# Kernel optimization log

Measured on AMD Instinct MI355X. Metric: run time of the kernel, lower is better.

## Reference

```python
import jax, jax.numpy as jnp
import numpy as np

N, E, D, R = 50000, 800000, 64, 65


def setup_inputs() -> dict:
    key = jax.random.key(0)
    ks = jax.random.split(key, 8)
    x = jax.random.normal(ks[0], (N, D), dtype=jnp.float32)
    src = jax.random.randint(ks[1], (E,), 0, N, dtype=jnp.int32)
    dst = jax.random.randint(ks[2], (E,), 0, N, dtype=jnp.int32)
    edge_type = jax.random.randint(ks[3], (E,), 0, R, dtype=jnp.int32)
    s = 1.0 / np.sqrt(D)
    W1 = jax.random.normal(ks[4], (R, D, D), dtype=jnp.float32) * s
    Wl1 = jax.random.normal(ks[5], (D, D), dtype=jnp.float32) * s
    W2 = jax.random.normal(ks[6], (R, D, D), dtype=jnp.float32) * s
    Wl2 = jax.random.normal(ks[7], (D, D), dtype=jnp.float32) * s
    return {"x": x, "src": src, "dst": dst, "edge_type": edge_type,
            "W1": W1, "Wl1": Wl1, "W2": W2, "Wl2": Wl2}


def _rgcn_layer(x, src, dst, edge_type, W, Wl):
    # x: [N, D_in], W: [R, D_in, D_out], Wl: [D_in, D_out]
    n = x.shape[0]
    r = W.shape[0]
    # per-relation transform of all node features: [R, N, D_out]
    xw = jnp.einsum('nd,rdh->rnh', x, W)
    # gather transformed source feature for each edge by its relation: [E, D_out]
    msg = xw[edge_type, src]
    # mean aggregation per (destination node, relation) as in PyG RGCNConv
    key = dst.astype(jnp.int32) * r + edge_type
    cnt = jax.ops.segment_sum(jnp.ones(key.shape, x.dtype), key, num_segments=n * r)
    norm = 1.0 / jnp.maximum(cnt[key], 1.0)  # [E]
    agg = jax.ops.segment_sum(msg * norm[:, None], dst, num_segments=n)  # [N, D_out]
    # self-loop linear term (self_loop_weights in original module)
    out = agg + x @ Wl
    # activation; dropout is identity in eval mode; batch norm disabled
    return jax.nn.relu(out)


def reference(x, src, dst, edge_type, W1, Wl1, W2, Wl2):
    h = _rgcn_layer(x, src, dst, edge_type, W1, Wl1)
    h = _rgcn_layer(h, src, dst, edge_type, W2, Wl2)
    return h
```

## Files before the change

kernel.cpp:

```cpp
#include <hip/hip_runtime.h>

typedef __attribute__((ext_vector_type(8))) short bf16x8;
typedef __attribute__((ext_vector_type(4))) float f32x4;
typedef __attribute__((ext_vector_type(2))) unsigned int u32x2;

constexpr int D = 64;
constexpr int SEG = 64;
constexpr int CSTR = 16;
constexpr int SBS = 1024;

__device__ inline unsigned short f2bf(float f) {
  unsigned u = __float_as_uint(f);
  u += 0x7fff + ((u >> 16) & 1);
  return (unsigned short)(u >> 16);
}
__device__ inline float bflo(unsigned u) { return __uint_as_float(u << 16); }
__device__ inline float bfhi(unsigned u) { return __uint_as_float(u & 0xffff0000u); }

__global__ __launch_bounds__(SBS) void count_kernel(
    const int* __restrict__ dst, const int* __restrict__ et,
    int* __restrict__ bcnt, int* __restrict__ deg, int E, int R, int nbE) {
  __shared__ int lh[128];
  int t = threadIdx.x;
  if (t < 128) lh[t] = 0;
  __syncthreads();
  int e = blockIdx.x * SBS + t;
  if (e < E) {
    atomicAdd(&deg[(long)dst[e] * CSTR], 1);
    atomicAdd(&lh[et[e]], 1);
  }
  __syncthreads();
  if (t < R) bcnt[t * nbE + blockIdx.x] = lh[t];
}

__global__ __launch_bounds__(256) void scanA_dual_kernel(
    const int* __restrict__ bcnt, const int* __restrict__ deg,
    int* __restrict__ bsum, int nBC, int N, int nbBC) {
  __shared__ int s[256];
  int t = threadIdx.x;
  int b = blockIdx.x;
  int v;
  if (b < nbBC) {
    int i = b * 256 + t;
    v = (i < nBC) ? bcnt[i] : 0;
  } else {
    int i = (b - nbBC) * 256 + t;
    v = (i < N) ? deg[(long)i * CSTR] : 0;
  }
  s[t] = v;
  __syncthreads();
  for (int o = 128; o > 0; o >>= 1) {
    if (t < o) s[t] += s[t + o];
    __syncthreads();
  }
  if (t == 0) bsum[b] = s[0];
}

__device__ inline void scanB_region(int* bsum, int nb, int t) {
  __shared__ int s[256];
  __shared__ int carry;
  if (t == 0) carry = 0;
  __syncthreads();
  for (int base = 0; base < nb; base += 256) {
    int i = base + t;
    int v = (i < nb) ? bsum[i] : 0;
    s[t] = v;
    __syncthreads();
    for (int o = 1; o < 256; o <<= 1) {
      int u = (t >= o) ? s[t - o] : 0;
      __syncthreads();
      s[t] += u;
      __syncthreads();
    }
    if (i < nb) bsum[i] = carry + s[t] - v;
    __syncthreads();
    if (t == 0) carry += s[255];
    __syncthreads();
  }
}

__global__ __launch_bounds__(256) void scanB_dual_kernel(
    int* __restrict__ bsum, int nbBC, int nbN) {
  int t = threadIdx.x;
  scanB_region(bsum, nbBC, t);
  scanB_region(bsum + nbBC, nbN, t);
}

__global__ __launch_bounds__(256) void scanC_dual_kernel(
    const int* __restrict__ bcnt, const int* __restrict__ deg,
    const int* __restrict__ bsum, int* __restrict__ prefE,
    int* __restrict__ dstoff, int* __restrict__ cur2,
    int nBC, int N, int nbBC) {
  __shared__ int s[256];
  int t = threadIdx.x;
  int b = blockIdx.x;
  bool isBC = (b < nbBC);
  int i = (isBC ? b : b - nbBC) * 256 + t;
  int n = isBC ? nBC : N;
  int v = 0;
  if (i < n) v = isBC ? bcnt[i] : deg[(long)i * CSTR];
  s[t] = v;
  __syncthreads();
  for (int o = 1; o < 256; o <<= 1) {
    int u = (t >= o) ? s[t - o] : 0;
    __syncthreads();
    s[t] += u;
    __syncthreads();
  }
  int excl = bsum[b] + s[t] - v;
  if (isBC) {
    if (i < n) prefE[i] = excl;
    if (i == n - 1) prefE[n] = excl + v;
  } else {
    if (i < n) { dstoff[i] = excl; cur2[(long)i * CSTR] = excl; }
    if (i == n - 1) dstoff[n] = excl + v;
  }
}

__global__ void prefix_wrel_kernel(const int* __restrict__ prefE,
                                   int* __restrict__ cursor, int* __restrict__ wrel,
                                   int2* __restrict__ eidx,
                                   int nbE, int R, int Ecap, int nwavesTot) {
  __shared__ int sc[128];
  int l = threadIdx.x;
  int tot = 0, c = 0;
  if (l < R) {
    tot = prefE[(l + 1) * nbE] - prefE[l * nbE];
    c = (tot + SEG - 1) & ~(SEG - 1);
  }
  sc[l] = c;
  __syncthreads();
  for (int ofs = 1; ofs < 128; ofs <<= 1) {
    int v = (l >= ofs) ? sc[l - ofs] : 0;
    __syncthreads();
    sc[l] += v;
    __syncthreads();
  }
  if (l < R) {
    int cur = sc[l] - c;
    cursor[l] = cur;
    int w0 = cur >> 6;
    int nw = c >> 6;
    for (int w = 0; w < nw; ++w) wrel[w0 + w] = l;
    for (int p = cur + tot; p < cur + c; ++p) eidx[p] = make_int2(-1, -1);
  }
  int total = sc[127];
  for (int p = total + l; p < Ecap; p += 128) eidx[p] = make_int2(-1, -1);
  for (int w = (total >> 6) + l; w < nwavesTot; w += 128) wrel[w] = 0;
}

__global__ __launch_bounds__(SBS) void scatter_kernel(
    const int* __restrict__ src, const int* __restrict__ dst, const int* __restrict__ et,
    const int* __restrict__ cursor, const int* __restrict__ prefE,
    int* __restrict__ cur2, int2* __restrict__ eidx,
    int E, int R, int nbE) {
  __shared__ int lh[128];
  __shared__ int lbase[128];
  __shared__ int lpre[128];
  __shared__ int sv[SBS];
  __shared__ int jv[SBS];
  __shared__ int rv[SBS];
  int t = threadIdx.x, b = blockIdx.x;
  if (t < 128) {
    lh[t] = 0;
    lbase[t] = (t < R) ? (cursor[t] + prefE[t * nbE + b] - prefE[t * nbE]) : 0;
  }
  __syncthreads();
  int e = b * SBS + t;
  bool valid = (e < E);
  int r = 0, s = 0, jd = 0, lr = 0;
  if (valid) {
    r = et[e]; s = src[e]; int d = dst[e];
    lr = atomicAdd(&lh[r], 1);
    jd = atomicAdd(&cur2[(long)d * CSTR], 1);
  }
  __syncthreads();
  if (t < 128) lpre[t] = lh[t];
  __syncthreads();
  for (int o = 1; o < 128; o <<= 1) {
    int u = (t >= o && t < 128) ? lpre[t - o] : 0;
    __syncthreads();
    if (t < 128) lpre[t] += u;
    __syncthreads();
  }
  if (valid) {
    int slot = (lpre[r] - lh[r]) + lr;
    sv[slot] = s; jv[slot] = jd; rv[slot] = r;
  }
  __syncthreads();
  int nvalid = min(E - b * SBS, SBS);
  if (t < nvalid) {
    int rr = rv[t];
    int ex = lpre[rr] - lh[rr];
    int pos = lbase[rr] + (t - ex);
    eidx[pos] = make_int2(sv[t], jv[t]);
  }
}

__global__ __launch_bounds__(256) void cvt_kernel(
    const float* __restrict__ x, unsigned short* __restrict__ xb, int nx, int nxb,
    const float* __restrict__ W1, unsigned short* __restrict__ WT1,
    const float* __restrict__ W2, unsigned short* __restrict__ WT2,
    const float* __restrict__ Wl1, unsigned short* __restrict__ WTl1,
    const float* __restrict__ Wl2, unsigned short* __restrict__ WTl2, int R) {
  const int b = blockIdx.x;
  const int t = threadIdx.x;
  if (b < nxb) {
    long i = ((long)b * 256 + t) * 8;
    if (i < nx) {
      float4 f0 = *(const float4*)(x + i);
      float4 f1 = *(const float4*)(x + i + 4);
      bf16x8 o;
      o[0] = (short)f2bf(f0.x); o[1] = (short)f2bf(f0.y);
      o[2] = (short)f2bf(f0.z); o[3] = (short)f2bf(f0.w);
      o[4] = (short)f2bf(f1.x); o[5] = (short)f2bf(f1.y);
      o[6] = (short)f2bf(f1.z); o[7] = (short)f2bf(f1.w);
      *(bf16x8*)(xb + i) = o;
    }
    return;
  }
  const int m = b - nxb;
  const float* Wsrc;
  unsigned short* Wdst;
  if (m < R)          { Wsrc = W1 + ((long)m << 12);        Wdst = WT1 + ((long)m << 12); }
  else if (m < 2 * R) { Wsrc = W2 + ((long)(m - R) << 12);  Wdst = WT2 + ((long)(m - R) << 12); }
  else if (m == 2 * R){ Wsrc = Wl1;                         Wdst = WTl1; }
  else                { Wsrc = Wl2;                         Wdst = WTl2; }
  __shared__ float tile[64][65];
#pragma unroll
  for (int it = 0; it < 16; ++it) {
    int idx = it * 256 + t;
    tile[idx >> 6][idx & 63] = Wsrc[idx];
  }
  __syncthreads();
#pragma unroll
  for (int it = 0; it < 16; ++it) {
    int j = it * 256 + t;
    Wdst[j] = f2bf(tile[j & 63][j >> 6]);
  }
}

__global__ __launch_bounds__(256)
void msg_kernel(const unsigned short* __restrict__ xb,
                const unsigned short* __restrict__ WT,
                const int2* __restrict__ eidx, const int* __restrict__ wrel,
                unsigned int* __restrict__ msgp, int* __restrict__ relrow, int nwaves) {
  const int lane = (int)threadIdx.x & 63;
  const int l15 = lane & 15;
  const int q = lane >> 4;
  const int nwg = (int)gridDim.x;
  const int bid = (int)blockIdx.x;
  const int xcd = bid & 7, idx = bid >> 3;
  const int qq = nwg >> 3, rr = nwg & 7;
  const int swz = (xcd < rr ? xcd * (qq + 1) : rr * (qq + 1) + (xcd - rr) * qq) + idx;
  const int wave = swz * 4 + ((int)threadIdx.x >> 6);
  if (wave >= nwaves) return;
  const long base = (long)wave * SEG;
  const int r = wrel[wave];
  const unsigned short* wb = WT + ((long)r << 12);
  int2 rec[4];
#pragma unroll
  for (int t = 0; t < 4; ++t) rec[t] = eidx[base + t * 16 + l15];
  bf16x8 Bf[4][2];
#pragma unroll
  for (int nt = 0; nt < 4; ++nt)
#pragma unroll
    for (int kh = 0; kh < 2; ++kh)
      Bf[nt][kh] = *(const bf16x8*)(wb + (nt * 16 + l15) * 64 + kh * 32 + q * 8);
  bf16x8 A[4][2];
#pragma unroll
  for (int t = 0; t < 4; ++t) {
    const unsigned short* xr = xb + ((long)max(rec[t].x, 0) << 6);
    A[t][0] = *(const bf16x8*)(xr + q * 8);
    A[t][1] = *(const bf16x8*)(xr + 32 + q * 8);
  }
  if (relrow) {
#pragma unroll
    for (int t = 0; t < 4; ++t)
      if (lane < 16 && rec[t].y >= 0) relrow[rec[t].y] = r;
  }
#pragma unroll
  for (int t = 0; t < 4; ++t) {
    f32x4 acc0 = (f32x4)0.0f, acc1 = (f32x4)0.0f, acc2 = (f32x4)0.0f, acc3 = (f32x4)0.0f;
    acc0 = __builtin_amdgcn_mfma_f32_16x16x32_bf16(A[t][0], Bf[0][0], acc0, 0, 0, 0);
    acc0 = __builtin_amdgcn_mfma_f32_16x16x32_bf16(A[t][1], Bf[0][1], acc0, 0, 0, 0);
    acc1 = __builtin_amdgcn_mfma_f32_16x16x32_bf16(A[t][0], Bf[1][0], acc1, 0, 0, 0);
    acc1 = __builtin_amdgcn_mfma_f32_16x16x32_bf16(A[t][1], Bf[1][1], acc1, 0, 0, 0);
    acc2 = __builtin_amdgcn_mfma_f32_16x16x32_bf16(A[t][0], Bf[2][0], acc2, 0, 0, 0);
    acc2 = __builtin_amdgcn_mfma_f32_16x16x32_bf16(A[t][1], Bf[2][1], acc2, 0, 0, 0);
    acc3 = __builtin_amdgcn_mfma_f32_16x16x32_bf16(A[t][0], Bf[3][0], acc3, 0, 0, 0);
    acc3 = __builtin_amdgcn_mfma_f32_16x16x32_bf16(A[t][1], Bf[3][1], acc3, 0, 0, 0);
#pragma unroll
    for (int rg = 0; rg < 4; ++rg) {
      int row = q * 4 + rg;
      int jd = __shfl(rec[t].y, row);
      if (jd >= 0) {
        unsigned p0 = (unsigned)f2bf(acc0[rg]) | ((unsigned)f2bf(acc1[rg]) << 16);
        unsigned p1 = (unsigned)f2bf(acc2[rg]) | ((unsigned)f2bf(acc3[rg]) << 16);
        u32x2 pk;
        pk.x = p0; pk.y = p1;
        *(u32x2*)(msgp + (long)jd * 32 + 2 * l15) = pk;
      }
    }
  }
}

__global__ __launch_bounds__(256) void weight_kernel(
    const int* __restrict__ relrow, const int* __restrict__ dstoff,
    float* __restrict__ wrow, int N) {
  __shared__ int rsh[4][256];
  const int wv = (int)threadIdx.x >> 6;
  const int lane = (int)threadIdx.x & 63;
  const int d = blockIdx.x * 4 + wv;
  if (d >= N) return;
  const int off = dstoff[d], end = dstoff[d + 1];
  const int deg = end - off;
  if (deg <= 0) return;
  if (deg <= 256) {
    const int nit = (deg + 63) >> 6;
    for (int it = 0; it < nit; ++it) {
      int l = it * 64 + lane;
      if (l < deg) rsh[wv][l] = relrow[off + l];
    }
    __threadfence_block();
    for (int it = 0; it < nit; ++it) {
      int l = it * 64 + lane;
      if (l < deg) {
        int rv = rsh[wv][l];
        int c = 0;
        for (int m = 0; m < deg; ++m) c += (rsh[wv][m] == rv) ? 1 : 0;
        wrow[off + l] = 1.0f / (float)c;
      }
    }
  } else {
    for (int l = lane; l < deg; l += 64) {
      int rv = relrow[off + l];
      int c = 0;
      for (int m = off; m < end; ++m) c += (relrow[m] == rv) ? 1 : 0;
      wrow[off + l] = 1.0f / (float)c;
    }
  }
}

__global__ __launch_bounds__(256) void aggsl_kernel(
    const unsigned int* __restrict__ msgp, const int* __restrict__ dstoff,
    const float* __restrict__ wrow,
    const unsigned short* __restrict__ xbin, const unsigned short* __restrict__ WTl,
    float* __restrict__ outp, unsigned short* __restrict__ hb, int N) {
  __shared__ float aggs[64][66];
  const int lane = (int)threadIdx.x & 63;
  const int wv = (int)threadIdx.x >> 6;
  const int base = blockIdx.x * 64;
  const int j = lane & 31;
  const int half = lane >> 5;
  for (int i16 = 0; i16 < 16; ++i16) {
    const int d = base + wv * 16 + i16;
    if (d >= N) break;
    const int off = dstoff[d], end = dstoff[d + 1];
    float a0 = 0.f, a1 = 0.f, b0 = 0.f, b1 = 0.f;
    float c0 = 0.f, c1 = 0.f, e0 = 0.f, e1 = 0.f;
    int i = off + half;
    for (; i + 6 < end; i += 8) {
      float w0 = wrow[i];
      float w1 = wrow[i + 2];
      float w2 = wrow[i + 4];
      float w3 = wrow[i + 6];
      unsigned u0 = msgp[(long)i * 32 + j];
      unsigned u1 = msgp[(long)(i + 2) * 32 + j];
      unsigned u2 = msgp[(long)(i + 4) * 32 + j];
      unsigned u3 = msgp[(long)(i + 6) * 32 + j];
      a0 = fmaf(w0, bflo(u0), a0);
      a1 = fmaf(w0, bfhi(u0), a1);
      b0 = fmaf(w1, bflo(u1), b0);
      b1 = fmaf(w1, bfhi(u1), b1);
      c0 = fmaf(w2, bflo(u2), c0);
      c1 = fmaf(w2, bfhi(u2), c1);
      e0 = fmaf(w3, bflo(u3), e0);
      e1 = fmaf(w3, bfhi(u3), e1);
    }
    for (; i + 2 < end; i += 4) {
      float w0 = wrow[i];
      float w1 = wrow[i + 2];
      unsigned u0 = msgp[(long)i * 32 + j];
      unsigned u1 = msgp[(long)(i + 2) * 32 + j];
      a0 = fmaf(w0, bflo(u0), a0);
      a1 = fmaf(w0, bfhi(u0), a1);
      b0 = fmaf(w1, bflo(u1), b0);
      b1 = fmaf(w1, bfhi(u1), b1);
    }
    if (i < end) {
      float w0 = wrow[i];
      unsigned u0 = msgp[(long)i * 32 + j];
      a0 = fmaf(w0, bflo(u0), a0);
      a1 = fmaf(w0, bfhi(u0), a1);
    }
    float aLo = (a0 + b0) + (c0 + e0), aHi = (a1 + b1) + (c1 + e1);
    aLo += __shfl_xor(aLo, 32);
    aHi += __shfl_xor(aHi, 32);
    if (half == 0) {
      const int k = j >> 1;
      const int colLo = (j & 1) ? 32 + k : k;
      aggs[d - base][colLo] = aLo;
      aggs[d - base][colLo + 16] = aHi;
    }
  }
  __syncthreads();
  const int l15 = lane & 15;
  const int q = lane >> 4;
  const int row0 = base + wv * 16;
  if (row0 >= N) return;
  bf16x8 Bf[4][2];
#pragma unroll
  for (int nt = 0; nt < 4; ++nt)
#pragma unroll
    for (int kh = 0; kh < 2; ++kh)
      Bf[nt][kh] = *(const bf16x8*)(WTl + (nt * 16 + l15) * 64 + kh * 32 + q * 8);
  const int m = min(row0 + l15, N - 1);
  const unsigned short* xr = xbin + ((long)m << 6);
  bf16x8 A0 = *(const bf16x8*)(xr + q * 8);
  bf16x8 A1 = *(const bf16x8*)(xr + 32 + q * 8);
  f32x4 acc[4];
#pragma unroll
  for (int nt = 0; nt < 4; ++nt)
#pragma unroll
    for (int rg = 0; rg < 4; ++rg) {
      int node = row0 + q * 4 + rg;
      acc[nt][rg] = (node < N) ? aggs[wv * 16 + q * 4 + rg][nt * 16 + l15] : 0.0f;
    }
#pragma unroll
  for (int nt = 0; nt < 4; ++nt) {
    acc[nt] = __builtin_amdgcn_mfma_f32_16x16x32_bf16(A0, Bf[nt][0], acc[nt], 0, 0, 0);
    acc[nt] = __builtin_amdgcn_mfma_f32_16x16x32_bf16(A1, Bf[nt][1], acc[nt], 0, 0, 0);
  }
#pragma unroll
  for (int rg = 0; rg < 4; ++rg) {
    int node = row0 + q * 4 + rg;
    if (node < N) {
#pragma unroll
      for (int nt = 0; nt < 4; ++nt) {
        float v = fmaxf(acc[nt][rg], 0.0f);
        if (outp) outp[(long)node * D + nt * 16 + l15] = v;
        if (hb) hb[(long)node * D + nt * 16 + l15] = f2bf(v);
      }
    }
  }
}

extern "C" void kernel_launch(void* const* d_in, const int* in_sizes, int n_in,
                              void* d_out, int out_size, void* d_ws, size_t ws_size,
                              hipStream_t stream) {
  const float* x   = (const float*)d_in[0];
  const int* src   = (const int*)d_in[1];
  const int* dst   = (const int*)d_in[2];
  const int* et    = (const int*)d_in[3];
  const float* W1  = (const float*)d_in[4];
  const float* Wl1 = (const float*)d_in[5];
  const float* W2  = (const float*)d_in[6];
  const float* Wl2 = (const float*)d_in[7];
  float* out = (float*)d_out;

  const int N = in_sizes[0] / D;
  const int E = in_sizes[1];
  const int R = in_sizes[4] / (D * D);

  const int Ecap = ((E + SEG - 1) & ~(SEG - 1)) + R * SEG;
  const int nwaves = Ecap / SEG;
  const int nbN = (N + 255) / 256;
  const int nbE = (E + SBS - 1) / SBS;
  const int nBC = R * nbE;
  const int nbBC = (nBC + 255) / 256;

  char* ws = (char*)d_ws;
  size_t off = 0;
  auto alloc = [&](size_t bytes) -> void* {
    void* p = (void*)(ws + off);
    off += (bytes + 255) & ~(size_t)255;
    return p;
  };
  int*   cursor = (int*)alloc((size_t)R * sizeof(int));
  int*   deg    = (int*)alloc((size_t)N * CSTR * sizeof(int));
  int*   cur2   = (int*)alloc((size_t)N * CSTR * sizeof(int));
  int*   bcnt   = (int*)alloc((size_t)nBC * sizeof(int));
  int*   prefE  = (int*)alloc((size_t)(nBC + 1) * sizeof(int));
  int*   bsum   = (int*)alloc((size_t)(nbBC + nbN) * sizeof(int));
  int*   dstoff = (int*)alloc((size_t)(N + 1) * sizeof(int));
  int*   relrow = (int*)alloc((size_t)E * sizeof(int));
  float* wrow   = (float*)alloc((size_t)E * sizeof(float));
  int*   wrel   = (int*)alloc((size_t)nwaves * sizeof(int));
  int2*  eidx   = (int2*)alloc((size_t)(Ecap + SEG) * sizeof(int2));
  unsigned int* msgp = (unsigned int*)alloc((size_t)E * 32 * sizeof(unsigned int));
  unsigned short* xb  = (unsigned short*)alloc((size_t)N * D * sizeof(unsigned short));
  unsigned short* hb  = (unsigned short*)alloc((size_t)N * D * sizeof(unsigned short));
  unsigned short* WT1 = (unsigned short*)alloc((size_t)R * D * D * sizeof(unsigned short));
  unsigned short* WT2 = (unsigned short*)alloc((size_t)R * D * D * sizeof(unsigned short));
  unsigned short* WTl1 = (unsigned short*)alloc((size_t)D * D * sizeof(unsigned short));
  unsigned short* WTl2 = (unsigned short*)alloc((size_t)D * D * sizeof(unsigned short));
  (void)ws_size; (void)n_in; (void)out_size;

  const int msg_blocks = (nwaves + 3) / 4;
  const int w_blocks = (N + 3) / 4;
  const int aggsl_blocks = (N + 63) / 64;
  const int nx = N * D;
  const int nxb = (nx + 2047) / 2048;
  const int cvt_blocks = nxb + 2 * R + 2;

  hipMemsetAsync(deg, 0, (size_t)N * CSTR * sizeof(int), stream);
  count_kernel<<<nbE, SBS, 0, stream>>>(dst, et, bcnt, deg, E, R, nbE);
  scanA_dual_kernel<<<nbBC + nbN, 256, 0, stream>>>(bcnt, deg, bsum, nBC, N, nbBC);
  scanB_dual_kernel<<<1, 256, 0, stream>>>(bsum, nbBC, nbN);
  scanC_dual_kernel<<<nbBC + nbN, 256, 0, stream>>>(bcnt, deg, bsum, prefE,
                                                    dstoff, cur2, nBC, N, nbBC);
  prefix_wrel_kernel<<<1, 128, 0, stream>>>(prefE, cursor, wrel, eidx,
                                            nbE, R, Ecap, nwaves);
  scatter_kernel<<<nbE, SBS, 0, stream>>>(src, dst, et, cursor, prefE, cur2,
                                          eidx, E, R, nbE);
  cvt_kernel<<<cvt_blocks, 256, 0, stream>>>(
      x, xb, nx, nxb, W1, WT1, W2, WT2, Wl1, WTl1, Wl2, WTl2, R);

  msg_kernel<<<msg_blocks, 256, 0, stream>>>(xb, WT1, eidx, wrel, msgp, relrow, nwaves);
  weight_kernel<<<w_blocks, 256, 0, stream>>>(relrow, dstoff, wrow, N);
  aggsl_kernel<<<aggsl_blocks, 256, 0, stream>>>(msgp, dstoff, wrow, xb, WTl1,
                                                 nullptr, hb, N);

  msg_kernel<<<msg_blocks, 256, 0, stream>>>(hb, WT2, eidx, wrel, msgp, nullptr, nwaves);
  aggsl_kernel<<<aggsl_blocks, 256, 0, stream>>>(msgp, dstoff, wrow, hb, WTl2,
                                                 out, nullptr, N);
}
```

Measured before the change: 326.9 us.

## Fuse setup kernels: merge count+convert, prefix into scatter, weights into aggregation

Folds the bf16 conversion of x and the weights into the count kernel launch, moves the per-relation prefix/wrel/padding setup into every scatter block (each block recomputes the scan redundantly), and computes the per-(dst,relation) mean weights inside the first aggregation kernel instead of a separate weight kernel. This removes three kernel launches and one pass over relrow/wrow. In exchange, every scatter block repeats a small scan, and the weight computation now sits on the aggregation critical path, where it adds shared memory use per block.

```diff
diff --git a/kernel.cpp b/kernel.cpp
--- a/kernel.cpp
+++ b/kernel.cpp
@@ -17,20 +17,63 @@
 __device__ inline float bflo(unsigned u) { return __uint_as_float(u << 16); }
 __device__ inline float bfhi(unsigned u) { return __uint_as_float(u & 0xffff0000u); }
 
-__global__ __launch_bounds__(SBS) void count_kernel(
+__global__ __launch_bounds__(SBS) void count_cvt_kernel(
     const int* __restrict__ dst, const int* __restrict__ et,
-    int* __restrict__ bcnt, int* __restrict__ deg, int E, int R, int nbE) {
-  __shared__ int lh[128];
+    int* __restrict__ bcnt, int* __restrict__ deg, int E, int R, int nbE,
+    const float* __restrict__ x, unsigned short* __restrict__ xb, int nx, int nxb,
+    const float* __restrict__ W1, unsigned short* __restrict__ WT1,
+    const float* __restrict__ W2, unsigned short* __restrict__ WT2,
+    const float* __restrict__ Wl1, unsigned short* __restrict__ WTl1,
+    const float* __restrict__ Wl2, unsigned short* __restrict__ WTl2) {
+  int b = blockIdx.x;
   int t = threadIdx.x;
-  if (t < 128) lh[t] = 0;
-  __syncthreads();
-  int e = blockIdx.x * SBS + t;
-  if (e < E) {
-    atomicAdd(&deg[(long)dst[e] * CSTR], 1);
-    atomicAdd(&lh[et[e]], 1);
-  }
-  __syncthreads();
-  if (t < R) bcnt[t * nbE + blockIdx.x] = lh[t];
+  if (b < nbE) {
+    __shared__ int lh[128];
+    if (t < 128) lh[t] = 0;
+    __syncthreads();
+    int e = b * SBS + t;
+    if (e < E) {
+      atomicAdd(&deg[(long)dst[e] * CSTR], 1);
+      atomicAdd(&lh[et[e]], 1);
+    }
+    __syncthreads();
+    if (t < R) bcnt[t * nbE + b] = lh[t];
+    return;
+  }
+  b -= nbE;
+  if (b < nxb) {
+    long i = ((long)b * SBS + t) * 8;
+    if (i < nx) {
+      float4 f0 = *(const float4*)(x + i);
+      float4 f1 = *(const float4*)(x + i + 4);
+      bf16x8 o;
+      o[0] = (short)f2bf(f0.x); o[1] = (short)f2bf(f0.y);
+      o[2] = (short)f2bf(f0.z); o[3] = (short)f2bf(f0.w);
+      o[4] = (short)f2bf(f1.x); o[5] = (short)f2bf(f1.y);
+      o[6] = (short)f2bf(f1.z); o[7] = (short)f2bf(f1.w);
+      *(bf16x8*)(xb + i) = o;
+    }
+    return;
+  }
+  const int m = b - nxb;
+  const float* Wsrc;
+  unsigned short* Wdst;
+  if (m < R)          { Wsrc = W1 + ((long)m << 12);        Wdst = WT1 + ((long)m << 12); }
+  else if (m < 2 * R) { Wsrc = W2 + ((long)(m - R) << 12);  Wdst = WT2 + ((long)(m - R) << 12); }
+  else if (m == 2 * R){ Wsrc = Wl1;                         Wdst = WTl1; }
+  else                { Wsrc = Wl2;                         Wdst = WTl2; }
+  __shared__ float tile[64][65];
+#pragma unroll
+  for (int it = 0; it < 4; ++it) {
+    int idx = it * SBS + t;
+    tile[idx >> 6][idx & 63] = Wsrc[idx];
+  }
+  __syncthreads();
+#pragma unroll
+  for (int it = 0; it < 4; ++it) {
+    int j = it * SBS + t;
+    Wdst[j] = f2bf(tile[j & 63][j >> 6]);
+  }
 }
 
 __global__ __launch_bounds__(256) void scanA_dual_kernel(
@@ -117,55 +160,55 @@
   }
 }
 
-__global__ void prefix_wrel_kernel(const int* __restrict__ prefE,
-                                   int* __restrict__ cursor, int* __restrict__ wrel,
-                                   int2* __restrict__ eidx,
-                                   int nbE, int R, int Ecap, int nwavesTot) {
-  __shared__ int sc[128];
-  int l = threadIdx.x;
-  int tot = 0, c = 0;
-  if (l < R) {
-    tot = prefE[(l + 1) * nbE] - prefE[l * nbE];
-    c = (tot + SEG - 1) & ~(SEG - 1);
-  }
-  sc[l] = c;
-  __syncthreads();
-  for (int ofs = 1; ofs < 128; ofs <<= 1) {
-    int v = (l >= ofs) ? sc[l - ofs] : 0;
-    __syncthreads();
-    sc[l] += v;
-    __syncthreads();
-  }
-  if (l < R) {
-    int cur = sc[l] - c;
-    cursor[l] = cur;
-    int w0 = cur >> 6;
-    int nw = c >> 6;
-    for (int w = 0; w < nw; ++w) wrel[w0 + w] = l;
-    for (int p = cur + tot; p < cur + c; ++p) eidx[p] = make_int2(-1, -1);
-  }
-  int total = sc[127];
-  for (int p = total + l; p < Ecap; p += 128) eidx[p] = make_int2(-1, -1);
-  for (int w = (total >> 6) + l; w < nwavesTot; w += 128) wrel[w] = 0;
-}
-
 __global__ __launch_bounds__(SBS) void scatter_kernel(
     const int* __restrict__ src, const int* __restrict__ dst, const int* __restrict__ et,
-    const int* __restrict__ cursor, const int* __restrict__ prefE,
-    int* __restrict__ cur2, int2* __restrict__ eidx,
-    int E, int R, int nbE) {
+    const int* __restrict__ prefE, int* __restrict__ cur2,
+    int2* __restrict__ eidx, int* __restrict__ wrel,
+    int E, int R, int nbE, int Ecap, int nwavesTot) {
   __shared__ int lh[128];
   __shared__ int lbase[128];
   __shared__ int lpre[128];
+  __shared__ int scur[128];
+  __shared__ int stot[128];
   __shared__ int sv[SBS];
   __shared__ int jv[SBS];
   __shared__ int rv[SBS];
   int t = threadIdx.x, b = blockIdx.x;
+  int myc = 0, mytot = 0;
   if (t < 128) {
+    if (t < R) {
+      mytot = prefE[(t + 1) * nbE] - prefE[t * nbE];
+      myc = (mytot + SEG - 1) & ~(SEG - 1);
+    }
+    lpre[t] = myc;
+  }
+  __syncthreads();
+  for (int o = 1; o < 128; o <<= 1) {
+    int u = (t >= o && t < 128) ? lpre[t - o] : 0;
+    __syncthreads();
+    if (t < 128) lpre[t] += u;
+    __syncthreads();
+  }
+  if (t < 128) {
+    scur[t] = lpre[t] - myc;
+    stot[t] = mytot;
     lh[t] = 0;
-    lbase[t] = (t < R) ? (cursor[t] + prefE[t * nbE + b] - prefE[t * nbE]) : 0;
-  }
-  __syncthreads();
+    lbase[t] = (t < R) ? (scur[t] + prefE[t * nbE + b] - prefE[t * nbE]) : 0;
+  }
+  __syncthreads();
+  for (int rr = b; rr <= R; rr += nbE) {
+    if (rr < R) {
+      int cur = scur[rr], tot = stot[rr];
+      int c = (tot + SEG - 1) & ~(SEG - 1);
+      for (int p = cur + tot + t; p < cur + c; p += SBS) eidx[p] = make_int2(-1, -1);
+      int w0 = cur >> 6, nw2 = c >> 6;
+      for (int w = t; w < nw2; w += SBS) wrel[w0 + w] = rr;
+    } else {
+      int total = scur[127];
+      for (int p = total + t; p < Ecap; p += SBS) eidx[p] = make_int2(-1, -1);
+      for (int w = (total >> 6) + t; w < nwavesTot; w += SBS) wrel[w] = 0;
+    }
+  }
   int e = b * SBS + t;
   bool valid = (e < E);
   int r = 0, s = 0, jd = 0, lr = 0;
@@ -190,53 +233,10 @@
   __syncthreads();
   int nvalid = min(E - b * SBS, SBS);
   if (t < nvalid) {
-    int rr = rv[t];
-    int ex = lpre[rr] - lh[rr];
-    int pos = lbase[rr] + (t - ex);
+    int rr2 = rv[t];
+    int ex = lpre[rr2] - lh[rr2];
+    int pos = lbase[rr2] + (t - ex);
     eidx[pos] = make_int2(sv[t], jv[t]);
-  }
-}
-
-__global__ __launch_bounds__(256) void cvt_kernel(
-    const float* __restrict__ x, unsigned short* __restrict__ xb, int nx, int nxb,
-    const float* __restrict__ W1, unsigned short* __restrict__ WT1,
-    const float* __restrict__ W2, unsigned short* __restrict__ WT2,
-    const float* __restrict__ Wl1, unsigned short* __restrict__ WTl1,
-    const float* __restrict__ Wl2, unsigned short* __restrict__ WTl2, int R) {
-  const int b = blockIdx.x;
-  const int t = threadIdx.x;
-  if (b < nxb) {
-    long i = ((long)b * 256 + t) * 8;
-    if (i < nx) {
-      float4 f0 = *(const float4*)(x + i);
-      float4 f1 = *(const float4*)(x + i + 4);
-      bf16x8 o;
-      o[0] = (short)f2bf(f0.x); o[1] = (short)f2bf(f0.y);
-      o[2] = (short)f2bf(f0.z); o[3] = (short)f2bf(f0.w);
-      o[4] = (short)f2bf(f1.x); o[5] = (short)f2bf(f1.y);
-      o[6] = (short)f2bf(f1.z); o[7] = (short)f2bf(f1.w);
-      *(bf16x8*)(xb + i) = o;
-    }
-    return;
-  }
-  const int m = b - nxb;
-  const float* Wsrc;
-  unsigned short* Wdst;
-  if (m < R)          { Wsrc = W1 + ((long)m << 12);        Wdst = WT1 + ((long)m << 12); }
-  else if (m < 2 * R) { Wsrc = W2 + ((long)(m - R) << 12);  Wdst = WT2 + ((long)(m - R) << 12); }
-  else if (m == 2 * R){ Wsrc = Wl1;                         Wdst = WTl1; }
-  else                { Wsrc = Wl2;                         Wdst = WTl2; }
-  __shared__ float tile[64][65];
-#pragma unroll
-  for (int it = 0; it < 16; ++it) {
-    int idx = it * 256 + t;
-    tile[idx >> 6][idx & 63] = Wsrc[idx];
-  }
-  __syncthreads();
-#pragma unroll
-  for (int it = 0; it < 16; ++it) {
-    int j = it * 256 + t;
-    Wdst[j] = f2bf(tile[j & 63][j >> 6]);
   }
 }
 
@@ -305,46 +305,10 @@
   }
 }
 
-__global__ __launch_bounds__(256) void weight_kernel(
-    const int* __restrict__ relrow, const int* __restrict__ dstoff,
-    float* __restrict__ wrow, int N) {
-  __shared__ int rsh[4][256];
-  const int wv = (int)threadIdx.x >> 6;
-  const int lane = (int)threadIdx.x & 63;
-  const int d = blockIdx.x * 4 + wv;
-  if (d >= N) return;
-  const int off = dstoff[d], end = dstoff[d + 1];
-  const int deg = end - off;
-  if (deg <= 0) return;
-  if (deg <= 256) {
-    const int nit = (deg + 63) >> 6;
-    for (int it = 0; it < nit; ++it) {
-      int l = it * 64 + lane;
-      if (l < deg) rsh[wv][l] = relrow[off + l];
-    }
-    __threadfence_block();
-    for (int it = 0; it < nit; ++it) {
-      int l = it * 64 + lane;
-      if (l < deg) {
-        int rv = rsh[wv][l];
-        int c = 0;
-        for (int m = 0; m < deg; ++m) c += (rsh[wv][m] == rv) ? 1 : 0;
-        wrow[off + l] = 1.0f / (float)c;
-      }
-    }
-  } else {
-    for (int l = lane; l < deg; l += 64) {
-      int rv = relrow[off + l];
-      int c = 0;
-      for (int m = off; m < end; ++m) c += (relrow[m] == rv) ? 1 : 0;
-      wrow[off + l] = 1.0f / (float)c;
-    }
-  }
-}
-
+template <bool CW>
 __global__ __launch_bounds__(256) void aggsl_kernel(
     const unsigned int* __restrict__ msgp, const int* __restrict__ dstoff,
-    const float* __restrict__ wrow,
+    const int* __restrict__ relrow, float* __restrict__ wrow,
     const unsigned short* __restrict__ xbin, const unsigned short* __restrict__ WTl,
     float* __restrict__ outp, unsigned short* __restrict__ hb, int N) {
   __shared__ float aggs[64][66];
@@ -357,44 +321,108 @@
     const int d = base + wv * 16 + i16;
     if (d >= N) break;
     const int off = dstoff[d], end = dstoff[d + 1];
-    float a0 = 0.f, a1 = 0.f, b0 = 0.f, b1 = 0.f;
-    float c0 = 0.f, c1 = 0.f, e0 = 0.f, e1 = 0.f;
-    int i = off + half;
-    for (; i + 6 < end; i += 8) {
-      float w0 = wrow[i];
-      float w1 = wrow[i + 2];
-      float w2 = wrow[i + 4];
-      float w3 = wrow[i + 6];
-      unsigned u0 = msgp[(long)i * 32 + j];
-      unsigned u1 = msgp[(long)(i + 2) * 32 + j];
-      unsigned u2 = msgp[(long)(i + 4) * 32 + j];
-      unsigned u3 = msgp[(long)(i + 6) * 32 + j];
-      a0 = fmaf(w0, bflo(u0), a0);
-      a1 = fmaf(w0, bfhi(u0), a1);
-      b0 = fmaf(w1, bflo(u1), b0);
-      b1 = fmaf(w1, bfhi(u1), b1);
-      c0 = fmaf(w2, bflo(u2), c0);
-      c1 = fmaf(w2, bfhi(u2), c1);
-      e0 = fmaf(w3, bflo(u3), e0);
-      e1 = fmaf(w3, bfhi(u3), e1);
-    }
-    for (; i + 2 < end; i += 4) {
-      float w0 = wrow[i];
-      float w1 = wrow[i + 2];
-      unsigned u0 = msgp[(long)i * 32 + j];
-      unsigned u1 = msgp[(long)(i + 2) * 32 + j];
-      a0 = fmaf(w0, bflo(u0), a0);
-      a1 = fmaf(w0, bfhi(u0), a1);
-      b0 = fmaf(w1, bflo(u1), b0);
-      b1 = fmaf(w1, bfhi(u1), b1);
-    }
-    if (i < end) {
-      float w0 = wrow[i];
-      unsigned u0 = msgp[(long)i * 32 + j];
-      a0 = fmaf(w0, bflo(u0), a0);
-      a1 = fmaf(w0, bfhi(u0), a1);
-    }
-    float aLo = (a0 + b0) + (c0 + e0), aHi = (a1 + b1) + (c1 + e1);
+    const int deg = end - off;
+    float f00 = 0.f, f01 = 0.f, f10 = 0.f, f11 = 0.f;
+    float f20 = 0.f, f21 = 0.f, f30 = 0.f, f31 = 0.f;
+    if constexpr (CW) {
+      __shared__ int rsh[4][256];
+      __shared__ int rsh2[4][256];
+      float* wsh = (float*)rsh[wv];
+      for (int c1 = 0; c1 < deg; c1 += 256) {
+        const int n1 = min(256, deg - c1);
+        for (int l = lane; l < n1; l += 64) rsh[wv][l] = relrow[off + c1 + l];
+        __threadfence_block();
+        int myrel[4], cnt[4];
+#pragma unroll
+        for (int k = 0; k < 4; ++k) {
+          int l = k * 64 + lane;
+          myrel[k] = (l < n1) ? rsh[wv][l] : -1;
+          cnt[k] = 0;
+        }
+        for (int c2 = 0; c2 < deg; c2 += 256) {
+          const int n2 = min(256, deg - c2);
+          const int* rr2;
+          if (c2 == c1) {
+            rr2 = rsh[wv];
+          } else {
+            for (int l = lane; l < n2; l += 64) rsh2[wv][l] = relrow[off + c2 + l];
+            __threadfence_block();
+            rr2 = rsh2[wv];
+          }
+          for (int mm = 0; mm < n2; ++mm) {
+            int rvv = rr2[mm];
+#pragma unroll
+            for (int k = 0; k < 4; ++k) cnt[k] += (rvv == myrel[k]) ? 1 : 0;
+          }
+        }
+        __threadfence_block();
+#pragma unroll
+        for (int k = 0; k < 4; ++k) {
+          int l = k * 64 + lane;
+          if (l < n1) {
+            float w = 1.0f / (float)cnt[k];
+            wsh[l] = w;
+            wrow[off + c1 + l] = w;
+          }
+        }
+        __threadfence_block();
+        const long gb = (long)off + c1;
+        int i = half;
+        for (; i + 6 < n1; i += 8) {
+          float w0 = wsh[i], w1 = wsh[i + 2], w2 = wsh[i + 4], w3 = wsh[i + 6];
+          unsigned u0 = msgp[(gb + i) * 32 + j];
+          unsigned u1 = msgp[(gb + i + 2) * 32 + j];
+          unsigned u2 = msgp[(gb + i + 4) * 32 + j];
+          unsigned u3 = msgp[(gb + i + 6) * 32 + j];
+          f00 = fmaf(w0, bflo(u0), f00); f01 = fmaf(w0, bfhi(u0), f01);
+          f10 = fmaf(w1, bflo(u1), f10); f11 = fmaf(w1, bfhi(u1), f11);
+          f20 = fmaf(w2, bflo(u2), f20); f21 = fmaf(w2, bfhi(u2), f21);
+          f30 = fmaf(w3, bflo(u3), f30); f31 = fmaf(w3, bfhi(u3), f31);
+        }
+        for (; i + 2 < n1; i += 4) {
+          float w0 = wsh[i], w1 = wsh[i + 2];
+          unsigned u0 = msgp[(gb + i) * 32 + j];
+          unsigned u1 = msgp[(gb + i + 2) * 32 + j];
+          f00 = fmaf(w0, bflo(u0), f00); f01 = fmaf(w0, bfhi(u0), f01);
+          f10 = fmaf(w1, bflo(u1), f10); f11 = fmaf(w1, bfhi(u1), f11);
+        }
+        if (i < n1) {
+          float w0 = wsh[i];
+          unsigned u0 = msgp[(gb + i) * 32 + j];
+          f00 = fmaf(w0, bflo(u0), f00); f01 = fmaf(w0, bfhi(u0), f01);
+        }
+      }
+    } else {
+      int i = off + half;
+      for (; i + 6 < end; i += 8) {
+        float w0 = wrow[i];
+        float w1 = wrow[i + 2];
+        float w2 = wrow[i + 4];
+        float w3 = wrow[i + 6];
+        unsigned u0 = msgp[(long)i * 32 + j];
+        unsigned u1 = msgp[(long)(i + 2) * 32 + j];
+        unsigned u2 = msgp[(long)(i + 4) * 32 + j];
+        unsigned u3 = msgp[(long)(i + 6) * 32 + j];
+        f00 = fmaf(w0, bflo(u0), f00); f01 = fmaf(w0, bfhi(u0), f01);
+        f10 = fmaf(w1, bflo(u1), f10); f11 = fmaf(w1, bfhi(u1), f11);
+        f20 = fmaf(w2, bflo(u2), f20); f21 = fmaf(w2, bfhi(u2), f21);
+        f30 = fmaf(w3, bflo(u3), f30); f31 = fmaf(w3, bfhi(u3), f31);
+      }
+      for (; i + 2 < end; i += 4) {
+        float w0 = wrow[i];
+        float w1 = wrow[i + 2];
+        unsigned u0 = msgp[(long)i * 32 + j];
+        unsigned u1 = msgp[(long)(i + 2) * 32 + j];
+        f00 = fmaf(w0, bflo(u0), f00); f01 = fmaf(w0, bfhi(u0), f01);
+        f10 = fmaf(w1, bflo(u1), f10); f11 = fmaf(w1, bfhi(u1), f11);
+      }
+      if (i < end) {
+        float w0 = wrow[i];
+        unsigned u0 = msgp[(long)i * 32 + j];
+        f00 = fmaf(w0, bflo(u0), f00); f01 = fmaf(w0, bfhi(u0), f01);
+      }
+    }
+    float aLo = (f00 + f10) + (f20 + f30), aHi = (f01 + f11) + (f21 + f31);
     aLo += __shfl_xor(aLo, 32);
     aHi += __shfl_xor(aHi, 32);
     if (half == 0) {
@@ -477,7 +505,6 @@
     off += (bytes + 255) & ~(size_t)255;
     return p;
   };
-  int*   cursor = (int*)alloc((size_t)R * sizeof(int));
   int*   deg    = (int*)alloc((size_t)N * CSTR * sizeof(int));
   int*   cur2   = (int*)alloc((size_t)N * CSTR * sizeof(int));
   int*   bcnt   = (int*)alloc((size_t)nBC * sizeof(int));
@@ -498,31 +525,27 @@
   (void)ws_size; (void)n_in; (void)out_size;
 
   const int msg_blocks = (nwaves + 3) / 4;
-  const int w_blocks = (N + 3) / 4;
   const int aggsl_blocks = (N + 63) / 64;
   const int nx = N * D;
-  const int nxb = (nx + 2047) / 2048;
-  const int cvt_blocks = nxb + 2 * R + 2;
+  const int nxb = (nx + SBS * 8 - 1) / (SBS * 8);
+  const int cc_blocks = nbE + nxb + 2 * R + 2;
 
   hipMemsetAsync(deg, 0, (size_t)N * CSTR * sizeof(int), stream);
-  count_kernel<<<nbE, SBS, 0, stream>>>(dst, et, bcnt, deg, E, R, nbE);
+  count_cvt_kernel<<<cc_blocks, SBS, 0, stream>>>(
+      dst, et, bcnt, deg, E, R, nbE,
+      x, xb, nx, nxb, W1, WT1, W2, WT2, Wl1, WTl1, Wl2, WTl2);
   scanA_dual_kernel<<<nbBC + nbN, 256, 0, stream>>>(bcnt, deg, bsum, nBC, N, nbBC);
   scanB_dual_kernel<<<1, 256, 0, stream>>>(bsum, nbBC, nbN);
   scanC_dual_kernel<<<nbBC + nbN, 256, 0, stream>>>(bcnt, deg, bsum, prefE,
                                                     dstoff, cur2, nBC, N, nbBC);
-  prefix_wrel_kernel<<<1, 128, 0, stream>>>(prefE, cursor, wrel, eidx,
-                                            nbE, R, Ecap, nwaves);
-  scatter_kernel<<<nbE, SBS, 0, stream>>>(src, dst, et, cursor, prefE, cur2,
-                                          eidx, E, R, nbE);
-  cvt_kernel<<<cvt_blocks, 256, 0, stream>>>(
-      x, xb, nx, nxb, W1, WT1, W2, WT2, Wl1, WTl1, Wl2, WTl2, R);
+  scatter_kernel<<<nbE, SBS, 0, stream>>>(src, dst, et, prefE, cur2,
+                                          eidx, wrel, E, R, nbE, Ecap, nwaves);
 
   msg_kernel<<<msg_blocks, 256, 0, stream>>>(xb, WT1, eidx, wrel, msgp, relrow, nwaves);
-  weight_kernel<<<w_blocks, 256, 0, stream>>>(relrow, dstoff, wrow, N);
-  aggsl_kernel<<<aggsl_blocks, 256, 0, stream>>>(msgp, dstoff, wrow, xb, WTl1,
-                                                 nullptr, hb, N);
+  aggsl_kernel<true><<<aggsl_blocks, 256, 0, stream>>>(
+      msgp, dstoff, relrow, wrow, xb, WTl1, nullptr, hb, N);
 
   msg_kernel<<<msg_blocks, 256, 0, stream>>>(hb, WT2, eidx, wrel, msgp, nullptr, nwaves);
-  aggsl_kernel<<<aggsl_blocks, 256, 0, stream>>>(msgp, dstoff, wrow, hb, WTl2,
-                                                 out, nullptr, N);
-}
+  aggsl_kernel<false><<<aggsl_blocks, 256, 0, stream>>>(
+      msgp, dstoff, nullptr, wrow, hb, WTl2, out, nullptr, N);
+}
```

New measurement: 329.4 us. No clear change (+0.8%).
